# Performance work log

Hardware: AMD Instinct MI355X
Metric: run time of the kernel (lower is better)

The kernel has to match this reference:

```python
import jax, jax.numpy as jnp
import numpy as np

B, S, E, H = 4, 2048, 2048, 16
D = E // H  # head_dim = 128
MAX_LEN = 2048


def _make_freqs():
    # standard RoPE frequencies: theta = 10000^{-2i/D}
    inv_freq = 1.0 / (10000.0 ** (np.arange(0, D, 2, dtype=np.float32) / D))  # [D/2]
    t = np.arange(MAX_LEN, dtype=np.float32)
    ang = np.outer(t, inv_freq)  # [max_len, D/2]
    cos = ang.reshape(1, MAX_LEN, 1, D // 2)
    return jnp.asarray(np.cos(cos)), jnp.asarray(np.sin(cos))


def setup_inputs() -> dict:
    key = jax.random.key(0)
    ks = jax.random.split(key, 10)
    sc = 1.0 / np.sqrt(E)
    freqs_cos, freqs_sin = _make_freqs()
    return {
        "x": jax.random.normal(ks[0], (B, S, E), dtype=jnp.float32),
        "freqs_cos": freqs_cos,
        "freqs_sin": freqs_sin,
        "wq": jax.random.normal(ks[1], (E, E), dtype=jnp.float32) * sc,
        "bq": jax.random.normal(ks[2], (E,), dtype=jnp.float32) * 0.01,
        "wk": jax.random.normal(ks[3], (E, E), dtype=jnp.float32) * sc,
        "bk": jax.random.normal(ks[4], (E,), dtype=jnp.float32) * 0.01,
        "wv": jax.random.normal(ks[5], (E, E), dtype=jnp.float32) * sc,
        "bv": jax.random.normal(ks[6], (E,), dtype=jnp.float32) * 0.01,
        "wo": jax.random.normal(ks[7], (E, E), dtype=jnp.float32) * sc,
        "bo": jax.random.normal(ks[8], (E,), dtype=jnp.float32) * 0.01,
    }


def _rope(t, cos, sin):
    # t: [B, S, H, D]; complex multiply on interleaved (even, odd) pairs
    tr = t.reshape(*t.shape[:-1], -1, 2)  # [B,S,H,D/2,2]
    xr, xi = tr[..., 0], tr[..., 1]
    rr = xr * cos - xi * sin
    ri = xr * sin + xi * cos
    return jnp.stack([rr, ri], axis=-1).reshape(t.shape)


def reference(x, freqs_cos, freqs_sin, wq, bq, wk, bk, wv, bv, wo, bo):
    b, s, _ = x.shape
    q = (x @ wq.T + bq).reshape(b, s, H, D)
    k = (x @ wk.T + bk).reshape(b, s, H, D)
    v = (x @ wv.T + bv).reshape(b, s, H, D)
    cos, sin = freqs_cos[:, :s], freqs_sin[:, :s]
    q = _rope(q, cos, sin)
    k = _rope(k, cos, sin)
    # FAITHFUL to source: q,k,v stay [B,S,H,D], so matmul contracts over D
    # producing per-position head-head scores [B,S,H,H] (no transpose to BHSD).
    qk = jnp.einsum("bshd,bsgd->bshg", q, k) / jnp.sqrt(jnp.float32(D))
    att = jax.nn.softmax(qk, axis=-1)
    att_out = jnp.einsum("bshg,bsgd->bshd", att, v)  # [B,S,H,D]
    # torch: transpose(1,2).contiguous().view(B,S,-1) -> h-major flatten
    att_out = jnp.transpose(att_out, (0, 2, 1, 3)).reshape(b, s, -1)
    return att_out @ wo.T + bo
```

## Files before the change

### kernel.cpp

```cpp
#include <hip/hip_runtime.h>
#include <stdint.h>

typedef unsigned short u16t;
typedef __attribute__((ext_vector_type(8))) short frag8;
typedef __attribute__((ext_vector_type(4))) float facc4;

#define S_LEN 2048
#define E_DIM 2048

__device__ __forceinline__ u16t f2bf(float f) {
    union { float f; uint32_t u; } c; c.f = f;
    return (u16t)((c.u + 0x7fffu + ((c.u >> 16) & 1u)) >> 16);
}

__global__ __launch_bounds__(256) void cvt_kernel(const float* __restrict__ src,
                                                  u16t* __restrict__ dst, int n4) {
    int i = blockIdx.x * 256 + threadIdx.x;
    if (i >= n4) return;
    float4 v = ((const float4*)src)[i];
    ushort4 o;
    o.x = f2bf(v.x); o.y = f2bf(v.y); o.z = f2bf(v.z); o.w = f2bf(v.w);
    ((ushort4*)dst)[i] = o;
}

__device__ __forceinline__ void gldl16(const u16t* g, u16t* l) {
    __builtin_amdgcn_global_load_lds(
        (__attribute__((address_space(1))) void*)(g),
        (__attribute__((address_space(3))) void*)(l), 16, 0, 0);
}

__device__ __forceinline__ void gemm_core(const u16t* __restrict__ A,
                                          const u16t* __restrict__ Bw,
                                          u16t* As0, u16t* As1,
                                          u16t* Bs0, u16t* Bs1,
                                          facc4 acc[4][4]) {
    const int t    = threadIdx.x;
    const int lane = t & 63;
    const int wid  = t >> 6;
    const int m16  = lane & 15;
    const int quad = lane >> 4;
    const int wm   = (wid & 1) * 64;
    const int wn   = (wid >> 1) * 64;
    const size_t bm0 = (size_t)blockIdx.y * 128;
    const size_t bn0 = (size_t)blockIdx.x * 128;

#pragma unroll
    for (int i = 0; i < 4; ++i)
#pragma unroll
        for (int j = 0; j < 4; ++j) acc[i][j] = facc4{0.f, 0.f, 0.f, 0.f};

    const u16t* Ab = A + bm0 * E_DIM;
    const u16t* Bb = Bw + bn0 * E_DIM;

    const int e0 = wid * 512;
    const int e1 = 2048 + wid * 512;
    const int le0 = e0 + lane * 8, le1 = e1 + lane * 8;
    const int r0 = le0 >> 5, c0 = le0 & 31;
    const int r1 = le1 >> 5, c1 = le1 & 31;
    const size_t ga0 = (size_t)r0 * E_DIM + c0;
    const size_t ga1 = (size_t)r1 * E_DIM + c1;

    for (int k0 = 0; k0 < E_DIM; k0 += 64) {
        __syncthreads();
        gldl16(Ab + ga0 + k0,      As0 + e0);
        gldl16(Ab + ga1 + k0,      As0 + e1);
        gldl16(Ab + ga0 + k0 + 32, As1 + e0);
        gldl16(Ab + ga1 + k0 + 32, As1 + e1);
        gldl16(Bb + ga0 + k0,      Bs0 + e0);
        gldl16(Bb + ga1 + k0,      Bs0 + e1);
        gldl16(Bb + ga0 + k0 + 32, Bs1 + e0);
        gldl16(Bb + ga1 + k0 + 32, Bs1 + e1);
        __syncthreads();

#pragma unroll
        for (int h = 0; h < 2; ++h) {
            const u16t* Ah = h ? As1 : As0;
            const u16t* Bh = h ? Bs1 : Bs0;
            frag8 av[4], bv[4];
#pragma unroll
            for (int i = 0; i < 4; ++i)
                av[i] = *(const frag8*)(Ah + (wm + i * 16 + m16) * 32 + quad * 8);
#pragma unroll
            for (int j = 0; j < 4; ++j)
                bv[j] = *(const frag8*)(Bh + (wn + j * 16 + m16) * 32 + quad * 8);
#pragma unroll
            for (int i = 0; i < 4; ++i)
#pragma unroll
                for (int j = 0; j < 4; ++j)
                    acc[i][j] = __builtin_amdgcn_mfma_f32_16x16x32_bf16(
                        av[i], bv[j], acc[i][j], 0, 0, 0);
        }
    }
}

struct QkvArgs {
    const u16t* w[3];
    const float* bias[3];
    u16t* out[3];
};

__global__ __launch_bounds__(256, 2)
void qkv_gemm(const u16t* __restrict__ xb, QkvArgs args,
              const float* __restrict__ fcos, const float* __restrict__ fsin) {
    __shared__ u16t As0[128 * 32], As1[128 * 32];
    __shared__ u16t Bs0[128 * 32], Bs1[128 * 32];
    facc4 acc[4][4];
    const int z = blockIdx.z;
    gemm_core(xb, args.w[z], As0, As1, Bs0, Bs1, acc);

    const int t    = threadIdx.x;
    const int lane = t & 63;
    const int m16  = lane & 15;
    const int quad = lane >> 4;
    const int wid  = t >> 6;
    const int wm   = (wid & 1) * 64;
    const int wn   = (wid >> 1) * 64;
    const int bm0  = blockIdx.y * 128;
    const int bn0  = blockIdx.x * 128;
    const bool rope = (z < 2);
    u16t* out = args.out[z];
    const float* bias = args.bias[z];

#pragma unroll
    for (int i = 0; i < 4; ++i) {
#pragma unroll
        for (int j = 0; j < 4; ++j) {
            const int n = bn0 + wn + j * 16 + m16;
            const float bn_ = bias[n];
#pragma unroll
            for (int r = 0; r < 4; ++r) {
                const int m = bm0 + wm + i * 16 + quad * 4 + r;
                float v = acc[i][j][r] + bn_;
                const float part = __shfl_xor(v, 1, 64);
                if (rope) {
                    const int s = m & (S_LEN - 1);
                    const int p = (n & 127) >> 1;
                    const float cs = fcos[s * 64 + p];
                    const float sn = fsin[s * 64 + p];
                    v = (n & 1) ? (part * sn + v * cs) : (v * cs - part * sn);
                }
                out[(size_t)m * E_DIM + n] = f2bf(v);
            }
        }
    }
}

__global__ __launch_bounds__(256, 2)
void out_gemm(const u16t* __restrict__ sh, const u16t* __restrict__ wob,
              const float* __restrict__ bo, float* __restrict__ out) {
    __shared__ u16t As0[128 * 32], As1[128 * 32];
    __shared__ u16t Bs0[128 * 32], Bs1[128 * 32];
    facc4 acc[4][4];
    gemm_core(sh, wob, As0, As1, Bs0, Bs1, acc);

    const int t    = threadIdx.x;
    const int lane = t & 63;
    const int m16  = lane & 15;
    const int quad = lane >> 4;
    const int wid  = t >> 6;
    const int wm   = (wid & 1) * 64;
    const int wn   = (wid >> 1) * 64;
    const int bm0  = blockIdx.y * 128;
    const int bn0  = blockIdx.x * 128;

#pragma unroll
    for (int i = 0; i < 4; ++i) {
#pragma unroll
        for (int j = 0; j < 4; ++j) {
            const int n = bn0 + wn + j * 16 + m16;
            const float bn_ = bo[n];
#pragma unroll
            for (int r = 0; r < 4; ++r) {
                const int m = bm0 + wm + i * 16 + quad * 4 + r;
                out[(size_t)m * E_DIM + n] = acc[i][j][r] + bn_;
            }
        }
    }
}

__global__ __launch_bounds__(256)
void attn_kernel(const u16t* __restrict__ qb, const u16t* __restrict__ kb,
                 const u16t* __restrict__ vb, u16t* __restrict__ sh) {
    __shared__ u16t Vs[4][16 * 136];
    __shared__ u16t Pt[4][16 * 32];

    const int t    = threadIdx.x;
    const int wid  = t >> 6;
    const int lane = t & 63;
    const int m16  = lane & 15;
    const int quad = lane >> 4;
    const int tk   = blockIdx.x * 4 + wid;
    const int b    = tk >> 11;
    const int s    = tk & (S_LEN - 1);
    const size_t row = (size_t)tk * E_DIM;

    frag8 aq[4], ak[4];
    const u16t* qrow = qb + row + m16 * 128 + quad * 8;
    const u16t* krow = kb + row + m16 * 128 + quad * 8;
#pragma unroll
    for (int ks = 0; ks < 4; ++ks) {
        aq[ks] = *(const frag8*)(qrow + ks * 32);
        ak[ks] = *(const frag8*)(krow + ks * 32);
    }

    u16t* vs = Vs[wid];
#pragma unroll
    for (int c = 0; c < 4; ++c) {
        const int e  = c * 512 + lane * 8;
        const int vr = e >> 7, vc = e & 127;
        *(uint4*)(vs + vr * 136 + vc) = *(const uint4*)(vb + row + e);
    }

    facc4 sacc = facc4{0.f, 0.f, 0.f, 0.f};
#pragma unroll
    for (int ks = 0; ks < 4; ++ks)
        sacc = __builtin_amdgcn_mfma_f32_16x16x32_bf16(aq[ks], ak[ks], sacc, 0, 0, 0);

    float p[4], mx[4], sm[4];
#pragma unroll
    for (int r = 0; r < 4; ++r) { p[r] = sacc[r] * 0.08838834764831845f; mx[r] = p[r]; }
#pragma unroll
    for (int msk = 1; msk < 16; msk <<= 1)
#pragma unroll
        for (int r = 0; r < 4; ++r) mx[r] = fmaxf(mx[r], __shfl_xor(mx[r], msk, 64));
#pragma unroll
    for (int r = 0; r < 4; ++r) { p[r] = __expf(p[r] - mx[r]); sm[r] = p[r]; }
#pragma unroll
    for (int msk = 1; msk < 16; msk <<= 1)
#pragma unroll
        for (int r = 0; r < 4; ++r) sm[r] += __shfl_xor(sm[r], msk, 64);

    u16t* pt = Pt[wid];
#pragma unroll
    for (int r = 0; r < 4; ++r)
        pt[(quad * 4 + r) * 32 + m16] = f2bf(p[r] / sm[r]);
    *(uint2*)(pt + m16 * 32 + 16 + quad * 4) = uint2{0u, 0u};

    __syncthreads();

    const frag8 aP = *(const frag8*)(pt + m16 * 32 + quad * 8);

    facc4 oacc[8];
#pragma unroll
    for (int d = 0; d < 8; ++d) oacc[d] = facc4{0.f, 0.f, 0.f, 0.f};
#pragma unroll
    for (int dblk = 0; dblk < 8; ++dblk) {
        union { u16t u[8]; frag8 f; } bb;
#pragma unroll
        for (int j = 0; j < 8; ++j)
            bb.u[j] = vs[((quad * 8 + j) & 15) * 136 + dblk * 16 + m16];
        oacc[dblk] = __builtin_amdgcn_mfma_f32_16x16x32_bf16(aP, bb.f, oacc[dblk], 0, 0, 0);
    }

    const size_t base = ((size_t)b << 22) + (size_t)(s >> 4) * E_DIM
                      + (size_t)((s & 15) * 128);
#pragma unroll
    for (int dblk = 0; dblk < 8; ++dblk) {
        const int d = dblk * 16 + m16;
#pragma unroll
        for (int r = 0; r < 4; ++r) {
            const int h = quad * 4 + r;
            sh[base + ((size_t)h << 18) + d] = f2bf(oacc[dblk][r]);
        }
    }
}

extern "C" void kernel_launch(void* const* d_in, const int* in_sizes, int n_in,
                              void* d_out, int out_size, void* d_ws, size_t ws_size,
                              hipStream_t stream) {
    const float* x    = (const float*)d_in[0];
    const float* fcos = (const float*)d_in[1];
    const float* fsin = (const float*)d_in[2];
    const float* wq   = (const float*)d_in[3];
    const float* bq   = (const float*)d_in[4];
    const float* wk   = (const float*)d_in[5];
    const float* bk   = (const float*)d_in[6];
    const float* wv   = (const float*)d_in[7];
    const float* bv   = (const float*)d_in[8];
    const float* wo   = (const float*)d_in[9];
    const float* bo   = (const float*)d_in[10];
    float* out = (float*)d_out;

    char* ws = (char*)d_ws;
    u16t* xb  = (u16t*)(ws);
    u16t* qb  = (u16t*)(ws + 33554432ull);
    u16t* kb  = (u16t*)(ws + 67108864ull);
    u16t* vb  = (u16t*)(ws + 100663296ull);
    u16t* wqb = (u16t*)(ws + 134217728ull);
    u16t* wkb = (u16t*)(ws + 142606336ull);
    u16t* wvb = (u16t*)(ws + 150994944ull);
    u16t* wob = (u16t*)(ws + 159383552ull);

    cvt_kernel<<<16384, 256, 0, stream>>>(x, xb, 4194304);
    cvt_kernel<<<4096, 256, 0, stream>>>(wq, wqb, 1048576);
    cvt_kernel<<<4096, 256, 0, stream>>>(wk, wkb, 1048576);
    cvt_kernel<<<4096, 256, 0, stream>>>(wv, wvb, 1048576);
    cvt_kernel<<<4096, 256, 0, stream>>>(wo, wob, 1048576);

    QkvArgs qa;
    qa.w[0] = wqb; qa.w[1] = wkb; qa.w[2] = wvb;
    qa.bias[0] = bq; qa.bias[1] = bk; qa.bias[2] = bv;
    qa.out[0] = qb; qa.out[1] = kb; qa.out[2] = vb;
    qkv_gemm<<<dim3(16, 64, 3), 256, 0, stream>>>(xb, qa, fcos, fsin);

    attn_kernel<<<2048, 256, 0, stream>>>(qb, kb, vb, xb);

    out_gemm<<<dim3(16, 64), 256, 0, stream>>>(xb, wob, bo, out);
}
```

Measured before the change: 513.8 us.

## Rewrite GEMM core as 256x256 double-buffered pipeline with swizzled LDS

Replaces the 128x128 single-stage GEMM core with a 256x256 tile computed by 512 threads. Next-K tiles are prefetched into a second LDS buffer while the current one is consumed, using vmcnt waits and barriers in place of full syncthreads. The change also adds an XOR-swizzled LDS layout to avoid bank conflicts, MFMA priority hints, and a block-index swizzle for L2 locality. The goal is higher arithmetic intensity and overlap of loads with MFMA, at the cost of 128KB of LDS per block, more accumulator registers and fewer blocks per CU.

```diff
diff --git a/kernel.cpp b/kernel.cpp
--- a/kernel.cpp
+++ b/kernel.cpp
@@ -7,6 +7,7 @@
 
 #define S_LEN 2048
 #define E_DIM 2048
+#define LDSH  8192
 
 __device__ __forceinline__ u16t f2bf(float f) {
     union { float f; uint32_t u; } c; c.f = f;
@@ -29,68 +30,109 @@
         (__attribute__((address_space(3))) void*)(l), 16, 0, 0);
 }
 
-__device__ __forceinline__ void gemm_core(const u16t* __restrict__ A,
-                                          const u16t* __restrict__ Bw,
-                                          u16t* As0, u16t* As1,
-                                          u16t* Bs0, u16t* Bs1,
-                                          facc4 acc[4][4]) {
-    const int t    = threadIdx.x;
-    const int lane = t & 63;
-    const int wid  = t >> 6;
-    const int m16  = lane & 15;
-    const int quad = lane >> 4;
-    const int wm   = (wid & 1) * 64;
-    const int wn   = (wid >> 1) * 64;
-    const size_t bm0 = (size_t)blockIdx.y * 128;
-    const size_t bn0 = (size_t)blockIdx.x * 128;
-
-#pragma unroll
-    for (int i = 0; i < 4; ++i)
+__device__ __forceinline__ void gemm256(const u16t* __restrict__ A,
+                                        const u16t* __restrict__ B,
+                                        int bm0, int bn0,
+                                        u16t* lds, facc4 acc[8][4]) {
+    const int t     = threadIdx.x;
+    const int lane  = t & 63;
+    const int wid   = t >> 6;
+    const int m16   = lane & 15;
+    const int quad  = lane >> 4;
+    const int wid_m = wid >> 2;
+    const int wid_n = wid & 3;
+
+#pragma unroll
+    for (int i = 0; i < 8; ++i)
 #pragma unroll
         for (int j = 0; j < 4; ++j) acc[i][j] = facc4{0.f, 0.f, 0.f, 0.f};
 
-    const u16t* Ab = A + bm0 * E_DIM;
-    const u16t* Bb = Bw + bn0 * E_DIM;
-
-    const int e0 = wid * 512;
-    const int e1 = 2048 + wid * 512;
-    const int le0 = e0 + lane * 8, le1 = e1 + lane * 8;
-    const int r0 = le0 >> 5, c0 = le0 & 31;
-    const int r1 = le1 >> 5, c1 = le1 & 31;
-    const size_t ga0 = (size_t)r0 * E_DIM + c0;
-    const size_t ga1 = (size_t)r1 * E_DIM + c1;
-
-    for (int k0 = 0; k0 < E_DIM; k0 += 64) {
-        __syncthreads();
-        gldl16(Ab + ga0 + k0,      As0 + e0);
-        gldl16(Ab + ga1 + k0,      As0 + e1);
-        gldl16(Ab + ga0 + k0 + 32, As1 + e0);
-        gldl16(Ab + ga1 + k0 + 32, As1 + e1);
-        gldl16(Bb + ga0 + k0,      Bs0 + e0);
-        gldl16(Bb + ga1 + k0,      Bs0 + e1);
-        gldl16(Bb + ga0 + k0 + 32, Bs1 + e0);
-        gldl16(Bb + ga1 + k0 + 32, Bs1 + e1);
-        __syncthreads();
-
-#pragma unroll
-        for (int h = 0; h < 2; ++h) {
-            const u16t* Ah = h ? As1 : As0;
-            const u16t* Bh = h ? Bs1 : Bs0;
-            frag8 av[4], bv[4];
-#pragma unroll
-            for (int i = 0; i < 4; ++i)
-                av[i] = *(const frag8*)(Ah + (wm + i * 16 + m16) * 32 + quad * 8);
-#pragma unroll
-            for (int j = 0; j < 4; ++j)
-                bv[j] = *(const frag8*)(Bh + (wn + j * 16 + m16) * 32 + quad * 8);
-#pragma unroll
-            for (int i = 0; i < 4; ++i)
-#pragma unroll
-                for (int j = 0; j < 4; ++j)
-                    acc[i][j] = __builtin_amdgcn_mfma_f32_16x16x32_bf16(
-                        av[i], bv[j], acc[i][j], 0, 0, 0);
-        }
-    }
+    const int colA = (((wid_m << 2) + quad) ^ (m16 & 7)) << 3;
+    const int colB = ((((wid_n >> 1) << 2) + quad) ^ (m16 & 7)) << 3;
+    const int roA  = m16 * 64 + colA;
+    const int roB  = ((wid_n & 1) * 64 + m16) * 64 + colB;
+
+    const int cp    = (lane & 7) ^ (lane >> 3);
+    const int rgrp  = cp >> 2;
+    const int qq    = cp & 3;
+    const int line0 = wid * 8 + (lane >> 3);
+    const u16t* pA[2]; const u16t* pB[2]; int dOf[2];
+#pragma unroll
+    for (int ld = 0; ld < 2; ++ld) {
+        const int grow = rgrp * 128 + ld * 64 + line0;
+        pA[ld] = A + (size_t)(bm0 + grow) * E_DIM + qq * 8;
+        pB[ld] = B + (size_t)(bn0 + grow) * E_DIM + qq * 8;
+        dOf[ld] = (ld * 512 + wid * 64) * 8;
+    }
+
+#pragma unroll
+    for (int ld = 0; ld < 2; ++ld) gldl16(pA[ld],      lds +         dOf[ld]);
+#pragma unroll
+    for (int ld = 0; ld < 2; ++ld) gldl16(pB[ld],      lds + 16384 + dOf[ld]);
+#pragma unroll
+    for (int ld = 0; ld < 2; ++ld) gldl16(pA[ld] + 32, lds + LDSH  + dOf[ld]);
+#pragma unroll
+    for (int ld = 0; ld < 2; ++ld) gldl16(pB[ld] + 32, lds + 24576 + dOf[ld]);
+
+#define MFMA16(IB)                                                            \
+    __builtin_amdgcn_s_setprio(1);                                            \
+    _Pragma("unroll")                                                         \
+    for (int i = 0; i < 4; ++i)                                               \
+        _Pragma("unroll")                                                     \
+        for (int j = 0; j < 4; ++j)                                           \
+            acc[i + IB][j] = __builtin_amdgcn_mfma_f32_16x16x32_bf16(         \
+                av[i], bv[j], acc[i + IB][j], 0, 0, 0);                       \
+    __builtin_amdgcn_s_setprio(0);
+
+#pragma unroll 2
+    for (int t0 = 0; t0 < 32; ++t0) {
+        const u16t* Lc = lds + (t0 & 1) * 32768;
+        u16t* Ln       = lds + ((t0 & 1) ^ 1) * 32768;
+        const int kn   = (t0 < 31) ? (t0 + 1) * 64 : 0;
+        frag8 av[4], bv[4];
+
+        gldl16(pA[0] + kn, Ln + dOf[0]);
+        gldl16(pA[1] + kn, Ln + dOf[1]);
+        asm volatile("s_waitcnt vmcnt(6)" ::: "memory");
+        __builtin_amdgcn_s_barrier();
+#pragma unroll
+        for (int j = 0; j < 4; ++j) bv[j] = *(const frag8*)(Lc + 16384 + roB + j * 1024);
+#pragma unroll
+        for (int i = 0; i < 4; ++i) av[i] = *(const frag8*)(Lc + roA + i * 1024);
+        MFMA16(0)
+
+        gldl16(pB[0] + kn, Ln + 16384 + dOf[0]);
+        gldl16(pB[1] + kn, Ln + 16384 + dOf[1]);
+#pragma unroll
+        for (int i = 0; i < 4; ++i) av[i] = *(const frag8*)(Lc + roA + (i + 4) * 1024);
+        MFMA16(4)
+
+        gldl16(pA[0] + kn + 32, Ln + LDSH + dOf[0]);
+        gldl16(pA[1] + kn + 32, Ln + LDSH + dOf[1]);
+        asm volatile("s_waitcnt vmcnt(6)" ::: "memory");
+        __builtin_amdgcn_s_barrier();
+#pragma unroll
+        for (int j = 0; j < 4; ++j) bv[j] = *(const frag8*)(Lc + 24576 + roB + j * 1024);
+#pragma unroll
+        for (int i = 0; i < 4; ++i) av[i] = *(const frag8*)(Lc + LDSH + roA + i * 1024);
+        MFMA16(0)
+
+        gldl16(pB[0] + kn + 32, Ln + 24576 + dOf[0]);
+        gldl16(pB[1] + kn + 32, Ln + 24576 + dOf[1]);
+#pragma unroll
+        for (int i = 0; i < 4; ++i) av[i] = *(const frag8*)(Lc + LDSH + roA + (i + 4) * 1024);
+        MFMA16(4)
+    }
+#undef MFMA16
+
+    asm volatile("s_waitcnt vmcnt(0)" ::: "memory");
+}
+
+__device__ __forceinline__ void tile_swz(int& bm0, int& bn0) {
+    const int orig = blockIdx.y * 8 + blockIdx.x;
+    const int swz  = (orig & 7) * 32 + (orig >> 3);
+    bm0 = (swz >> 3) * 256;
+    bn0 = (swz & 7) * 256;
 }
 
 struct QkvArgs {
@@ -99,37 +141,35 @@
     u16t* out[3];
 };
 
-__global__ __launch_bounds__(256, 2)
+__global__ __launch_bounds__(512, 2)
 void qkv_gemm(const u16t* __restrict__ xb, QkvArgs args,
               const float* __restrict__ fcos, const float* __restrict__ fsin) {
-    __shared__ u16t As0[128 * 32], As1[128 * 32];
-    __shared__ u16t Bs0[128 * 32], Bs1[128 * 32];
-    facc4 acc[4][4];
+    __shared__ u16t lds[65536];
+    facc4 acc[8][4];
+    int bm0, bn0; tile_swz(bm0, bn0);
     const int z = blockIdx.z;
-    gemm_core(xb, args.w[z], As0, As1, Bs0, Bs1, acc);
-
-    const int t    = threadIdx.x;
-    const int lane = t & 63;
-    const int m16  = lane & 15;
-    const int quad = lane >> 4;
-    const int wid  = t >> 6;
-    const int wm   = (wid & 1) * 64;
-    const int wn   = (wid >> 1) * 64;
-    const int bm0  = blockIdx.y * 128;
-    const int bn0  = blockIdx.x * 128;
+    gemm256(xb, args.w[z], bm0, bn0, lds, acc);
+
+    const int t     = threadIdx.x;
+    const int lane  = t & 63;
+    const int m16   = lane & 15;
+    const int quad  = lane >> 4;
+    const int wid   = t >> 6;
+    const int wid_m = wid >> 2;
+    const int wid_n = wid & 3;
     const bool rope = (z < 2);
     u16t* out = args.out[z];
     const float* bias = args.bias[z];
 
 #pragma unroll
-    for (int i = 0; i < 4; ++i) {
+    for (int i = 0; i < 8; ++i) {
 #pragma unroll
         for (int j = 0; j < 4; ++j) {
-            const int n = bn0 + wn + j * 16 + m16;
+            const int n = bn0 + wid_n * 64 + j * 16 + m16;
             const float bn_ = bias[n];
 #pragma unroll
             for (int r = 0; r < 4; ++r) {
-                const int m = bm0 + wm + i * 16 + quad * 4 + r;
+                const int m = bm0 + wid_m * 128 + i * 16 + quad * 4 + r;
                 float v = acc[i][j][r] + bn_;
                 const float part = __shfl_xor(v, 1, 64);
                 if (rope) {
@@ -145,33 +185,31 @@
     }
 }
 
-__global__ __launch_bounds__(256, 2)
+__global__ __launch_bounds__(512, 2)
 void out_gemm(const u16t* __restrict__ sh, const u16t* __restrict__ wob,
               const float* __restrict__ bo, float* __restrict__ out) {
-    __shared__ u16t As0[128 * 32], As1[128 * 32];
-    __shared__ u16t Bs0[128 * 32], Bs1[128 * 32];
-    facc4 acc[4][4];
-    gemm_core(sh, wob, As0, As1, Bs0, Bs1, acc);
-
-    const int t    = threadIdx.x;
-    const int lane = t & 63;
-    const int m16  = lane & 15;
-    const int quad = lane >> 4;
-    const int wid  = t >> 6;
-    const int wm   = (wid & 1) * 64;
-    const int wn   = (wid >> 1) * 64;
-    const int bm0  = blockIdx.y * 128;
-    const int bn0  = blockIdx.x * 128;
-
-#pragma unroll
-    for (int i = 0; i < 4; ++i) {
+    __shared__ u16t lds[65536];
+    facc4 acc[8][4];
+    int bm0, bn0; tile_swz(bm0, bn0);
+    gemm256(sh, wob, bm0, bn0, lds, acc);
+
+    const int t     = threadIdx.x;
+    const int lane  = t & 63;
+    const int m16   = lane & 15;
+    const int quad  = lane >> 4;
+    const int wid   = t >> 6;
+    const int wid_m = wid >> 2;
+    const int wid_n = wid & 3;
+
+#pragma unroll
+    for (int i = 0; i < 8; ++i) {
 #pragma unroll
         for (int j = 0; j < 4; ++j) {
-            const int n = bn0 + wn + j * 16 + m16;
+            const int n = bn0 + wid_n * 64 + j * 16 + m16;
             const float bn_ = bo[n];
 #pragma unroll
             for (int r = 0; r < 4; ++r) {
-                const int m = bm0 + wm + i * 16 + quad * 4 + r;
+                const int m = bm0 + wid_m * 128 + i * 16 + quad * 4 + r;
                 out[(size_t)m * E_DIM + n] = acc[i][j][r] + bn_;
             }
         }
@@ -301,9 +339,9 @@
     qa.w[0] = wqb; qa.w[1] = wkb; qa.w[2] = wvb;
     qa.bias[0] = bq; qa.bias[1] = bk; qa.bias[2] = bv;
     qa.out[0] = qb; qa.out[1] = kb; qa.out[2] = vb;
-    qkv_gemm<<<dim3(16, 64, 3), 256, 0, stream>>>(xb, qa, fcos, fsin);
+    qkv_gemm<<<dim3(8, 32, 3), 512, 0, stream>>>(xb, qa, fcos, fsin);
 
     attn_kernel<<<2048, 256, 0, stream>>>(qb, kb, vb, xb);
 
-    out_gemm<<<dim3(16, 64), 256, 0, stream>>>(xb, wob, bo, out);
-}
+    out_gemm<<<dim3(8, 32), 512, 0, stream>>>(xb, wob, bo, out);
+}
```

Result: faster. 499.1 us (-2.9%).
